# Kernel optimization log

Measured on AMD Instinct MI355X. Metric: run time of the kernel, lower is better.

## Reference

```python
import jax, jax.numpy as jnp
from jax import lax
import numpy as np

H = 32  # LSTM hidden size


def setup_inputs() -> dict:
    key = jax.random.key(0)
    ks = jax.random.split(key, 10)
    B, T = 4096, 200
    s1 = 1.0 / np.sqrt(5)
    sl = 1.0 / np.sqrt(H)
    s2 = 1.0 / np.sqrt(H)
    return {
        "x": jax.random.normal(ks[0], (B, T, 5), dtype=jnp.float32),
        "fc1_w": jax.random.uniform(ks[1], (20, 5), jnp.float32, -s1, s1),
        "fc1_b": jax.random.uniform(ks[2], (20,), jnp.float32, -s1, s1),
        "w_ih": jax.random.uniform(ks[3], (4 * H, 20), jnp.float32, -sl, sl),
        "w_hh": jax.random.uniform(ks[4], (4 * H, H), jnp.float32, -sl, sl),
        "b_ih": jax.random.uniform(ks[5], (4 * H,), jnp.float32, -sl, sl),
        "b_hh": jax.random.uniform(ks[6], (4 * H,), jnp.float32, -sl, sl),
        "fc2_w": jax.random.uniform(ks[7], (2, H), jnp.float32, -s2, s2),
        "fc2_b": jax.random.uniform(ks[8], (2,), jnp.float32, -s2, s2),
    }


def reference(x, fc1_w, fc1_b, w_ih, w_hh, b_ih, b_hh, fc2_w, fc2_b):
    # fc1 + relu (dropout is identity in eval mode)
    h = jax.nn.relu(jnp.einsum("bti,oi->bto", x, fc1_w) + fc1_b)  # [B,T,20]
    B = x.shape[0]
    # Precompute input projections for all timesteps (one big GEMM)
    gx = jnp.einsum("bti,gi->btg", h, w_ih) + b_ih + b_hh  # [B,T,4H]
    gx = jnp.swapaxes(gx, 0, 1)  # [T,B,4H]

    def step(carry, gxt):
        h_prev, c_prev = carry
        gates = gxt + h_prev @ w_hh.T  # [B,4H]
        i, f, g, o = jnp.split(gates, 4, axis=-1)  # torch gate order i,f,g,o
        i = jax.nn.sigmoid(i)
        f = jax.nn.sigmoid(f)
        g = jnp.tanh(g)
        o = jax.nn.sigmoid(o)
        c = f * c_prev + i * g
        hn = o * jnp.tanh(c)
        return (hn, c), None

    zeros = jnp.zeros((B, H), dtype=x.dtype)
    (hT, _), _ = lax.scan(step, (zeros, zeros), gx)
    # fc2 on last timestep's hidden state
    return hT @ fc2_w.T + fc2_b  # [B,2]
```

## Files before the change

kernel.cpp:

```cpp
#include <hip/hip_runtime.h>

#define TT  200
#define IN  5
#define NH  32
#define FC1 20
#define CH  64
#define RS  12

typedef _Float16 h2t __attribute__((ext_vector_type(2)));
typedef _Float16 h4t __attribute__((ext_vector_type(4)));
typedef _Float16 h8t __attribute__((ext_vector_type(8)));

#if __has_builtin(__builtin_amdgcn_fdot2)
#define FDOT2(a, b, c) __builtin_amdgcn_fdot2((a), (b), (c), false)
#else
__device__ __forceinline__ float FDOT2(h2t a, h2t b, float c) {
    return fmaf((float)a.x, (float)b.x, fmaf((float)a.y, (float)b.y, c));
}
#endif

__device__ __forceinline__ float sigm(float a) {
    return __builtin_amdgcn_rcpf(1.f + __expf(-a));
}
__device__ __forceinline__ float tanh_f(float a) {
    return fmaf(2.f, __builtin_amdgcn_rcpf(1.f + __expf(-2.f * a)), -1.f);
}

#define EXT2(dst, src, i0, i1) dst = __builtin_shufflevector(src, src, i0, i1)

__global__ __attribute__((amdgpu_waves_per_eu(4, 4))) __launch_bounds__(64)
void lstm_fused(
    const float* __restrict__ x,
    const float* __restrict__ fc1_w,
    const float* __restrict__ fc1_b,
    const float* __restrict__ w_ih,
    const float* __restrict__ w_hh,
    const float* __restrict__ b_ih,
    const float* __restrict__ b_hh,
    const float* __restrict__ fc2_w,
    const float* __restrict__ fc2_b,
    float* __restrict__ out)
{
    const int b = blockIdx.x;
    const int l = threadIdx.x;
    const int u = l & 31;
    const int p = l >> 5;

    __shared__ __align__(16) h2t h20c[CH * RS];
    __shared__ __align__(16) _Float16 sh_h[NH];

    const int rA = u + 32 * p;
    const int rB = rA + 64;
    h2t wA[26], wB[26];
    {
        const float4* pa = (const float4*)(w_ih + rA * FC1);
        const float4* pb = (const float4*)(w_ih + rB * FC1);
        #pragma unroll
        for (int j = 0; j < 5; ++j) {
            float4 va = pa[j], vb = pb[j];
            wA[2*j]   = h2t{(_Float16)va.x, (_Float16)va.y};
            wA[2*j+1] = h2t{(_Float16)va.z, (_Float16)va.w};
            wB[2*j]   = h2t{(_Float16)vb.x, (_Float16)vb.y};
            wB[2*j+1] = h2t{(_Float16)vb.z, (_Float16)vb.w};
        }
        const float4* ca = (const float4*)(w_hh + rA * NH);
        const float4* cb = (const float4*)(w_hh + rB * NH);
        #pragma unroll
        for (int j = 0; j < 8; ++j) {
            float4 va = ca[j], vb = cb[j];
            wA[10+2*j]   = h2t{(_Float16)va.x, (_Float16)va.y};
            wA[10+2*j+1] = h2t{(_Float16)va.z, (_Float16)va.w};
            wB[10+2*j]   = h2t{(_Float16)vb.x, (_Float16)vb.y};
            wB[10+2*j+1] = h2t{(_Float16)vb.z, (_Float16)vb.w};
        }
    }
    const float biasA = b_ih[rA] + b_hh[rA];
    const float biasB = b_ih[rB] + b_hh[rB];

    const float An = (p == 0) ? 2.f : 1.f;
    const float Bn = (p == 0) ? -2.f : -1.f;
    const float Cn = (p == 0) ? -1.f : 0.f;

    if (l < 16) ((unsigned int*)sh_h)[l] = 0u;
    float c = 0.f;

    const float* xb = x + (size_t)b * (TT * IN);

    for (int tc = 0; tc < TT; tc += CH) {
        {
            const int t = tc + l;
            if (t < TT) {
                float xv[IN];
                #pragma unroll
                for (int i = 0; i < IN; ++i) xv[i] = xb[t * IN + i];
                h2t* row = h20c + (size_t)l * RS;
                #pragma unroll
                for (int j = 0; j < FC1; j += 2) {
                    float a0 = fc1_b[j], a1 = fc1_b[j + 1];
                    #pragma unroll
                    for (int i = 0; i < IN; ++i) {
                        a0 = fmaf(fc1_w[j * IN + i],       xv[i], a0);
                        a1 = fmaf(fc1_w[(j + 1) * IN + i], xv[i], a1);
                    }
                    row[j >> 1] = h2t{(_Float16)fmaxf(a0, 0.f),
                                      (_Float16)fmaxf(a1, 0.f)};
                }
            }
        }
        __syncthreads();

        const int te = (TT - tc < CH) ? (TT - tc) : CH;
        for (int k = 0; k < te; ++k) {
            h2t xin[26];
            {
                const h2t* row = h20c + (size_t)k * RS;
                h8t r0 = *(const h8t*)(row);
                h8t r1 = *(const h8t*)(row + 4);
                h4t r2 = *(const h4t*)(row + 8);
                EXT2(xin[0], r0, 0, 1);  EXT2(xin[1], r0, 2, 3);
                EXT2(xin[2], r0, 4, 5);  EXT2(xin[3], r0, 6, 7);
                EXT2(xin[4], r1, 0, 1);  EXT2(xin[5], r1, 2, 3);
                EXT2(xin[6], r1, 4, 5);  EXT2(xin[7], r1, 6, 7);
                EXT2(xin[8], r2, 0, 1);  EXT2(xin[9], r2, 2, 3);
                const h8t* hp = (const h8t*)sh_h;
                h8t h0 = hp[0], h1 = hp[1], h2 = hp[2], h3 = hp[3];
                EXT2(xin[10], h0, 0, 1); EXT2(xin[11], h0, 2, 3);
                EXT2(xin[12], h0, 4, 5); EXT2(xin[13], h0, 6, 7);
                EXT2(xin[14], h1, 0, 1); EXT2(xin[15], h1, 2, 3);
                EXT2(xin[16], h1, 4, 5); EXT2(xin[17], h1, 6, 7);
                EXT2(xin[18], h2, 0, 1); EXT2(xin[19], h2, 2, 3);
                EXT2(xin[20], h2, 4, 5); EXT2(xin[21], h2, 6, 7);
                EXT2(xin[22], h3, 0, 1); EXT2(xin[23], h3, 2, 3);
                EXT2(xin[24], h3, 4, 5); EXT2(xin[25], h3, 6, 7);
            }

            float aA0 = biasA, aA1 = 0.f, aB0 = biasB, aB1 = 0.f;
            #pragma unroll
            for (int j = 0; j < 26; j += 2) {
                aA0 = FDOT2(wA[j],     xin[j],     aA0);
                aA1 = FDOT2(wA[j + 1], xin[j + 1], aA1);
                aB0 = FDOT2(wB[j],     xin[j],     aB0);
                aB1 = FDOT2(wB[j + 1], xin[j + 1], aB1);
            }
            const float aA = aA0 + aA1;
            const float aB = aB0 + aB1;

            const float s0 = sigm(aA);
            const float e1 = __expf(Bn * aB);
            const float s1 = fmaf(An, __builtin_amdgcn_rcpf(1.f + e1), Cn);

            const float x0 = __shfl_xor(s0, 32);
            const float x1 = __shfl_xor(s1, 32);

            const float ig = (p == 0) ? (s0 * s1) : (x0 * x1);
            const float fv = (p == 0) ? x0 : s0;
            const float ov = (p == 0) ? x1 : s1;
            c = fmaf(fv, c, ig);
            const float hval = ov * tanh_f(c);

            if (p == 0) sh_h[u] = (_Float16)hval;
            __syncthreads();
        }
    }

    if (l < 2) {
        float acc = fc2_b[l];
        #pragma unroll
        for (int k = 0; k < NH; ++k)
            acc = fmaf(fc2_w[l * NH + k], (float)sh_h[k], acc);
        out[(size_t)b * 2 + l] = acc;
    }
}

extern "C" void kernel_launch(void* const* d_in, const int* in_sizes, int n_in,
                              void* d_out, int out_size, void* d_ws, size_t ws_size,
                              hipStream_t stream) {
    const float* x     = (const float*)d_in[0];
    const float* fc1_w = (const float*)d_in[1];
    const float* fc1_b = (const float*)d_in[2];
    const float* w_ih  = (const float*)d_in[3];
    const float* w_hh  = (const float*)d_in[4];
    const float* b_ih  = (const float*)d_in[5];
    const float* b_hh  = (const float*)d_in[6];
    const float* fc2_w = (const float*)d_in[7];
    const float* fc2_b = (const float*)d_in[8];
    float* out = (float*)d_out;

    const int B = in_sizes[0] / (TT * IN);
    lstm_fused<<<dim3(B), dim3(64), 0, stream>>>(
        x, fc1_w, fc1_b, w_ih, w_hh, b_ih, b_hh, fc2_w, fc2_b, out);
}
```

Before: 153.7 us.

## Prepack fp16 recurrent weights in a prep kernel and drop the per-step barrier

A small prep kernel converts w_ih and w_hh to packed fp16 pairs in a row-interleaved workspace layout. The main kernel then loads its per-thread weights with coalesced uint4 reads and no per-element conversion. The per-timestep __syncthreads is replaced by a compiler memory fence, which relies on the 64-thread block being a single wavefront so LDS accesses stay ordered. This adds a second kernel launch and depends on wave64 execution for correctness.

Result: no change. 154.3 us (+0.4%).

```diff
diff --git a/kernel.cpp b/kernel.cpp
--- a/kernel.cpp
+++ b/kernel.cpp
@@ -6,6 +6,7 @@
 #define FC1 20
 #define CH  64
 #define RS  12
+#define NG  7
 
 typedef _Float16 h2t __attribute__((ext_vector_type(2)));
 typedef _Float16 h4t __attribute__((ext_vector_type(4)));
@@ -28,13 +29,31 @@
 
 #define EXT2(dst, src, i0, i1) dst = __builtin_shufflevector(src, src, i0, i1)
 
+__global__ __launch_bounds__(256) void prep_w(
+    const float* __restrict__ w_ih, const float* __restrict__ w_hh,
+    unsigned int* __restrict__ ws)
+{
+    const int tid = blockIdx.x * 256 + threadIdx.x;
+    if (tid >= NG * 128 * 4) return;
+    const int q   = tid & 3;
+    const int rem = tid >> 2;
+    const int row = rem & 127;
+    const int g   = rem >> 7;
+    const int j   = 4 * g + q;
+    const int d0  = 2 * j;
+    float a = 0.f, b = 0.f;
+    if (d0 < FC1)      { a = w_ih[row * FC1 + d0];        b = w_ih[row * FC1 + d0 + 1]; }
+    else if (d0 < 52)  { a = w_hh[row * NH + d0 - FC1];   b = w_hh[row * NH + d0 - FC1 + 1]; }
+    h2t hv = { (_Float16)a, (_Float16)b };
+    ws[tid] = __builtin_bit_cast(unsigned int, hv);
+}
+
 __global__ __attribute__((amdgpu_waves_per_eu(4, 4))) __launch_bounds__(64)
 void lstm_fused(
     const float* __restrict__ x,
     const float* __restrict__ fc1_w,
     const float* __restrict__ fc1_b,
-    const float* __restrict__ w_ih,
-    const float* __restrict__ w_hh,
+    const unsigned int* __restrict__ wt,
     const float* __restrict__ b_ih,
     const float* __restrict__ b_hh,
     const float* __restrict__ fc2_w,
@@ -51,28 +70,29 @@
 
     const int rA = u + 32 * p;
     const int rB = rA + 64;
+
     h2t wA[26], wB[26];
     {
-        const float4* pa = (const float4*)(w_ih + rA * FC1);
-        const float4* pb = (const float4*)(w_ih + rB * FC1);
+        const uint4* wp = (const uint4*)wt;
         #pragma unroll
-        for (int j = 0; j < 5; ++j) {
-            float4 va = pa[j], vb = pb[j];
-            wA[2*j]   = h2t{(_Float16)va.x, (_Float16)va.y};
-            wA[2*j+1] = h2t{(_Float16)va.z, (_Float16)va.w};
-            wB[2*j]   = h2t{(_Float16)vb.x, (_Float16)vb.y};
-            wB[2*j+1] = h2t{(_Float16)vb.z, (_Float16)vb.w};
+        for (int g = 0; g < NG - 1; ++g) {
+            uint4 va = wp[g * 128 + rA];
+            uint4 vb = wp[g * 128 + rB];
+            wA[4*g+0] = __builtin_bit_cast(h2t, va.x);
+            wA[4*g+1] = __builtin_bit_cast(h2t, va.y);
+            wA[4*g+2] = __builtin_bit_cast(h2t, va.z);
+            wA[4*g+3] = __builtin_bit_cast(h2t, va.w);
+            wB[4*g+0] = __builtin_bit_cast(h2t, vb.x);
+            wB[4*g+1] = __builtin_bit_cast(h2t, vb.y);
+            wB[4*g+2] = __builtin_bit_cast(h2t, vb.z);
+            wB[4*g+3] = __builtin_bit_cast(h2t, vb.w);
         }
-        const float4* ca = (const float4*)(w_hh + rA * NH);
-        const float4* cb = (const float4*)(w_hh + rB * NH);
-        #pragma unroll
-        for (int j = 0; j < 8; ++j) {
-            float4 va = ca[j], vb = cb[j];
-            wA[10+2*j]   = h2t{(_Float16)va.x, (_Float16)va.y};
-            wA[10+2*j+1] = h2t{(_Float16)va.z, (_Float16)va.w};
-            wB[10+2*j]   = h2t{(_Float16)vb.x, (_Float16)vb.y};
-            wB[10+2*j+1] = h2t{(_Float16)vb.z, (_Float16)vb.w};
-        }
+        uint4 va = wp[6 * 128 + rA];
+        uint4 vb = wp[6 * 128 + rB];
+        wA[24] = __builtin_bit_cast(h2t, va.x);
+        wA[25] = __builtin_bit_cast(h2t, va.y);
+        wB[24] = __builtin_bit_cast(h2t, vb.x);
+        wB[25] = __builtin_bit_cast(h2t, vb.y);
     }
     const float biasA = b_ih[rA] + b_hh[rA];
     const float biasB = b_ih[rB] + b_hh[rB];
@@ -159,7 +179,7 @@
             const float hval = ov * tanh_f(c);
 
             if (p == 0) sh_h[u] = (_Float16)hval;
-            __syncthreads();
+            asm volatile("" ::: "memory");
         }
     }
 
@@ -185,8 +205,10 @@
     const float* fc2_w = (const float*)d_in[7];
     const float* fc2_b = (const float*)d_in[8];
     float* out = (float*)d_out;
+    unsigned int* ws = (unsigned int*)d_ws;
 
     const int B = in_sizes[0] / (TT * IN);
+    prep_w<<<dim3((NG * 128 * 4 + 255) / 256), dim3(256), 0, stream>>>(w_ih, w_hh, ws);
     lstm_fused<<<dim3(B), dim3(64), 0, stream>>>(
-        x, fc1_w, fc1_b, w_ih, w_hh, b_ih, b_hh, fc2_w, fc2_b, out);
-}
+        x, fc1_w, fc1_b, ws, b_ih, b_hh, fc2_w, fc2_b, out);
+}
```

## Precompute input gate projections per chunk and split recurrent dot across wave halves

Applied to the files above, without the earlier changes.

Moves the W_ih·fc1 projection out of the serial recurrence: each chunk of 16 timesteps is precomputed in parallel into shared memory, and a prep kernel repacks weights to fp16 in workspace. The recurrent step now has each lane compute a 16-wide partial dot for all four gates, combining halves through LDS instead of shuffles. Per-step __syncthreads is replaced by compiler barriers, relying on single-wave lockstep execution. This shortens the serial critical path per timestep, at the cost of an extra kernel launch and reliance on implicit wave synchronisation for LDS visibility.

Result: slower. 275.0 us (+78.9%).

```diff
diff --git a/kernel.cpp b/kernel.cpp
--- a/kernel.cpp
+++ b/kernel.cpp
@@ -4,12 +4,13 @@
 #define IN  5
 #define NH  32
 #define FC1 20
-#define CH  64
-#define RS  12
+#define CH  16
+
+#define WS_WHH  0
+#define WS_WIH  2048
+#define WS_BIAS 3584
 
 typedef _Float16 h2t __attribute__((ext_vector_type(2)));
-typedef _Float16 h4t __attribute__((ext_vector_type(4)));
-typedef _Float16 h8t __attribute__((ext_vector_type(8)));
 
 #if __has_builtin(__builtin_amdgcn_fdot2)
 #define FDOT2(a, b, c) __builtin_amdgcn_fdot2((a), (b), (c), false)
@@ -26,17 +27,43 @@
     return fmaf(2.f, __builtin_amdgcn_rcpf(1.f + __expf(-2.f * a)), -1.f);
 }
 
-#define EXT2(dst, src, i0, i1) dst = __builtin_shufflevector(src, src, i0, i1)
-
-__global__ __attribute__((amdgpu_waves_per_eu(4, 4))) __launch_bounds__(64)
-void lstm_fused(
+__device__ __forceinline__ h2t bc_h2(unsigned int v) {
+    return __builtin_bit_cast(h2t, v);
+}
+
+__global__ __launch_bounds__(256) void prep_w(
+    const float* __restrict__ w_ih, const float* __restrict__ w_hh,
+    const float* __restrict__ b_ih, const float* __restrict__ b_hh,
+    unsigned int* __restrict__ ws)
+{
+    const int tid = blockIdx.x * 256 + threadIdx.x;
+    if (tid < 2048) {
+        const int l = tid >> 5, k = tid & 31;
+        const int rp = k >> 3, j = k & 7;
+        const int row = (l & 31) + 32 * rp;
+        const int d0  = 16 * (l >> 5) + 2 * j;
+        h2t hv = { (_Float16)w_hh[row * NH + d0],
+                   (_Float16)w_hh[row * NH + d0 + 1] };
+        ws[WS_WHH + tid] = __builtin_bit_cast(unsigned int, hv);
+    } else if (tid < 3584) {
+        const int t = tid - 2048;
+        const int row = t / 12, j = t % 12;
+        const int d0 = 2 * j;
+        float a = 0.f, b = 0.f;
+        if (d0 < FC1) { a = w_ih[row * FC1 + d0]; b = w_ih[row * FC1 + d0 + 1]; }
+        h2t hv = { (_Float16)a, (_Float16)b };
+        ws[WS_WIH + (row * 12 + j)] = __builtin_bit_cast(unsigned int, hv);
+    } else if (tid < 3712) {
+        const int r = tid - 3584;
+        ((float*)(ws + WS_BIAS))[r] = b_ih[r] + b_hh[r];
+    }
+}
+
+__global__ __launch_bounds__(64) void lstm_fused(
     const float* __restrict__ x,
     const float* __restrict__ fc1_w,
     const float* __restrict__ fc1_b,
-    const float* __restrict__ w_ih,
-    const float* __restrict__ w_hh,
-    const float* __restrict__ b_ih,
-    const float* __restrict__ b_hh,
+    const unsigned int* __restrict__ ws,
     const float* __restrict__ fc2_w,
     const float* __restrict__ fc2_b,
     float* __restrict__ out)
@@ -46,54 +73,37 @@
     const int u = l & 31;
     const int p = l >> 5;
 
-    __shared__ __align__(16) h2t h20c[CH * RS];
+    __shared__ __align__(16) float4 gx[CH * 32];
+    __shared__ __align__(16) float4 dcomb[64];
     __shared__ __align__(16) _Float16 sh_h[NH];
 
-    const int rA = u + 32 * p;
-    const int rB = rA + 64;
-    h2t wA[26], wB[26];
+    h2t whh[32];
     {
-        const float4* pa = (const float4*)(w_ih + rA * FC1);
-        const float4* pb = (const float4*)(w_ih + rB * FC1);
+        const uint4* wp = (const uint4*)(ws + WS_WHH + l * 32);
         #pragma unroll
-        for (int j = 0; j < 5; ++j) {
-            float4 va = pa[j], vb = pb[j];
-            wA[2*j]   = h2t{(_Float16)va.x, (_Float16)va.y};
-            wA[2*j+1] = h2t{(_Float16)va.z, (_Float16)va.w};
-            wB[2*j]   = h2t{(_Float16)vb.x, (_Float16)vb.y};
-            wB[2*j+1] = h2t{(_Float16)vb.z, (_Float16)vb.w};
+        for (int g = 0; g < 8; ++g) {
+            uint4 v = wp[g];
+            whh[4*g+0] = bc_h2(v.x); whh[4*g+1] = bc_h2(v.y);
+            whh[4*g+2] = bc_h2(v.z); whh[4*g+3] = bc_h2(v.w);
         }
-        const float4* ca = (const float4*)(w_hh + rA * NH);
-        const float4* cb = (const float4*)(w_hh + rB * NH);
-        #pragma unroll
-        for (int j = 0; j < 8; ++j) {
-            float4 va = ca[j], vb = cb[j];
-            wA[10+2*j]   = h2t{(_Float16)va.x, (_Float16)va.y};
-            wA[10+2*j+1] = h2t{(_Float16)va.z, (_Float16)va.w};
-            wB[10+2*j]   = h2t{(_Float16)vb.x, (_Float16)vb.y};
-            wB[10+2*j+1] = h2t{(_Float16)vb.z, (_Float16)vb.w};
-        }
-    }
-    const float biasA = b_ih[rA] + b_hh[rA];
-    const float biasB = b_ih[rB] + b_hh[rB];
-
-    const float An = (p == 0) ? 2.f : 1.f;
-    const float Bn = (p == 0) ? -2.f : -1.f;
-    const float Cn = (p == 0) ? -1.f : 0.f;
+    }
 
     if (l < 16) ((unsigned int*)sh_h)[l] = 0u;
     float c = 0.f;
 
+    const int   tq = l & 15;
+    const int   q  = l >> 4;
     const float* xb = x + (size_t)b * (TT * IN);
+    const float* biasf = (const float*)(ws + WS_BIAS);
 
     for (int tc = 0; tc < TT; tc += CH) {
         {
-            const int t = tc + l;
+            const int t = tc + tq;
             if (t < TT) {
                 float xv[IN];
                 #pragma unroll
                 for (int i = 0; i < IN; ++i) xv[i] = xb[t * IN + i];
-                h2t* row = h20c + (size_t)l * RS;
+                h2t h20p[10];
                 #pragma unroll
                 for (int j = 0; j < FC1; j += 2) {
                     float a0 = fc1_b[j], a1 = fc1_b[j + 1];
@@ -102,8 +112,34 @@
                         a0 = fmaf(fc1_w[j * IN + i],       xv[i], a0);
                         a1 = fmaf(fc1_w[(j + 1) * IN + i], xv[i], a1);
                     }
-                    row[j >> 1] = h2t{(_Float16)fmaxf(a0, 0.f),
-                                      (_Float16)fmaxf(a1, 0.f)};
+                    h20p[j >> 1] = h2t{(_Float16)fmaxf(a0, 0.f),
+                                       (_Float16)fmaxf(a1, 0.f)};
+                }
+                #pragma unroll
+                for (int s = 0; s < 8; ++s) {
+                    const int uslot = 8 * q + s;
+                    float dacc[4];
+                    #pragma unroll
+                    for (int m = 0; m < 4; ++m) {
+                        const int row = uslot + 32 * m;
+                        const uint4* wr = (const uint4*)(ws + WS_WIH + row * 12);
+                        uint4 w0 = wr[0], w1 = wr[1];
+                        uint4 w2 = wr[2];
+                        float a0 = biasf[row], a1 = 0.f;
+                        a0 = FDOT2(bc_h2(w0.x), h20p[0], a0);
+                        a1 = FDOT2(bc_h2(w0.y), h20p[1], a1);
+                        a0 = FDOT2(bc_h2(w0.z), h20p[2], a0);
+                        a1 = FDOT2(bc_h2(w0.w), h20p[3], a1);
+                        a0 = FDOT2(bc_h2(w1.x), h20p[4], a0);
+                        a1 = FDOT2(bc_h2(w1.y), h20p[5], a1);
+                        a0 = FDOT2(bc_h2(w1.z), h20p[6], a0);
+                        a1 = FDOT2(bc_h2(w1.w), h20p[7], a1);
+                        a0 = FDOT2(bc_h2(w2.x), h20p[8], a0);
+                        a1 = FDOT2(bc_h2(w2.y), h20p[9], a1);
+                        dacc[m] = a0 + a1;
+                    }
+                    gx[tq * 32 + uslot] =
+                        make_float4(dacc[0], dacc[1], dacc[2], dacc[3]);
                 }
             }
         }
@@ -111,56 +147,48 @@
 
         const int te = (TT - tc < CH) ? (TT - tc) : CH;
         for (int k = 0; k < te; ++k) {
-            h2t xin[26];
+            const float4 g4 = gx[k * 32 + u];
+            const float sd0 = (p == 0) ? g4.x : 0.f;
+            const float sd1 = (p == 0) ? g4.y : 0.f;
+            const float sd2 = (p == 0) ? g4.z : 0.f;
+            const float sd3 = (p == 0) ? g4.w : 0.f;
+            h2t xin[8];
             {
-                const h2t* row = h20c + (size_t)k * RS;
-                h8t r0 = *(const h8t*)(row);
-                h8t r1 = *(const h8t*)(row + 4);
-                h4t r2 = *(const h4t*)(row + 8);
-                EXT2(xin[0], r0, 0, 1);  EXT2(xin[1], r0, 2, 3);
-                EXT2(xin[2], r0, 4, 5);  EXT2(xin[3], r0, 6, 7);
-                EXT2(xin[4], r1, 0, 1);  EXT2(xin[5], r1, 2, 3);
-                EXT2(xin[6], r1, 4, 5);  EXT2(xin[7], r1, 6, 7);
-                EXT2(xin[8], r2, 0, 1);  EXT2(xin[9], r2, 2, 3);
-                const h8t* hp = (const h8t*)sh_h;
-                h8t h0 = hp[0], h1 = hp[1], h2 = hp[2], h3 = hp[3];
-                EXT2(xin[10], h0, 0, 1); EXT2(xin[11], h0, 2, 3);
-                EXT2(xin[12], h0, 4, 5); EXT2(xin[13], h0, 6, 7);
-                EXT2(xin[14], h1, 0, 1); EXT2(xin[15], h1, 2, 3);
-                EXT2(xin[16], h1, 4, 5); EXT2(xin[17], h1, 6, 7);
-                EXT2(xin[18], h2, 0, 1); EXT2(xin[19], h2, 2, 3);
-                EXT2(xin[20], h2, 4, 5); EXT2(xin[21], h2, 6, 7);
-                EXT2(xin[22], h3, 0, 1); EXT2(xin[23], h3, 2, 3);
-                EXT2(xin[24], h3, 4, 5); EXT2(xin[25], h3, 6, 7);
+                const uint4* hp = (const uint4*)((const char*)sh_h + 32 * p);
+                uint4 h0 = hp[0], h1 = hp[1];
+                xin[0] = bc_h2(h0.x); xin[1] = bc_h2(h0.y);
+                xin[2] = bc_h2(h0.z); xin[3] = bc_h2(h0.w);
+                xin[4] = bc_h2(h1.x); xin[5] = bc_h2(h1.y);
+                xin[6] = bc_h2(h1.z); xin[7] = bc_h2(h1.w);
             }
-
-            float aA0 = biasA, aA1 = 0.f, aB0 = biasB, aB1 = 0.f;
+            float dA[4];
             #pragma unroll
-            for (int j = 0; j < 26; j += 2) {
-                aA0 = FDOT2(wA[j],     xin[j],     aA0);
-                aA1 = FDOT2(wA[j + 1], xin[j + 1], aA1);
-                aB0 = FDOT2(wB[j],     xin[j],     aB0);
-                aB1 = FDOT2(wB[j + 1], xin[j + 1], aB1);
+            for (int m = 0; m < 4; ++m) {
+                float a0 = (m == 0) ? sd0 : (m == 1) ? sd1 : (m == 2) ? sd2 : sd3;
+                float a1 = 0.f;
+                a0 = FDOT2(whh[8*m+0], xin[0], a0);
+                a1 = FDOT2(whh[8*m+1], xin[1], a1);
+                a0 = FDOT2(whh[8*m+2], xin[2], a0);
+                a1 = FDOT2(whh[8*m+3], xin[3], a1);
+                a0 = FDOT2(whh[8*m+4], xin[4], a0);
+                a1 = FDOT2(whh[8*m+5], xin[5], a1);
+                a0 = FDOT2(whh[8*m+6], xin[6], a0);
+                a1 = FDOT2(whh[8*m+7], xin[7], a1);
+                dA[m] = a0 + a1;
             }
-            const float aA = aA0 + aA1;
-            const float aB = aB0 + aB1;
-
-            const float s0 = sigm(aA);
-            const float e1 = __expf(Bn * aB);
-            const float s1 = fmaf(An, __builtin_amdgcn_rcpf(1.f + e1), Cn);
-
-            const float x0 = __shfl_xor(s0, 32);
-            const float x1 = __shfl_xor(s1, 32);
-
-            const float ig = (p == 0) ? (s0 * s1) : (x0 * x1);
-            const float fv = (p == 0) ? x0 : s0;
-            const float ov = (p == 0) ? x1 : s1;
-            c = fmaf(fv, c, ig);
-            const float hval = ov * tanh_f(c);
-
+            dcomb[l] = make_float4(dA[0], dA[1], dA[2], dA[3]);
+            asm volatile("" ::: "memory");
+            const float4 dp = dcomb[l ^ 32];
+            const float gi = sigm(dA[0] + dp.x);
+            const float gf = sigm(dA[1] + dp.y);
+            const float gg = tanh_f(dA[2] + dp.z);
+            const float go = sigm(dA[3] + dp.w);
+            c = fmaf(gf, c, gi * gg);
+            const float hval = go * tanh_f(c);
             if (p == 0) sh_h[u] = (_Float16)hval;
-            __syncthreads();
+            asm volatile("" ::: "memory");
         }
+        __syncthreads();
     }
 
     if (l < 2) {
@@ -185,8 +213,10 @@
     const float* fc2_w = (const float*)d_in[7];
     const float* fc2_b = (const float*)d_in[8];
     float* out = (float*)d_out;
+    unsigned int* ws = (unsigned int*)d_ws;
 
     const int B = in_sizes[0] / (TT * IN);
+    prep_w<<<dim3(15), dim3(256), 0, stream>>>(w_ih, w_hh, b_ih, b_hh, ws);
     lstm_fused<<<dim3(B), dim3(64), 0, stream>>>(
-        x, fc1_w, fc1_b, w_ih, w_hh, b_ih, b_hh, fc2_w, fc2_b, out);
-}
+        x, fc1_w, fc1_b, ws, fc2_w, fc2_b, out);
+}
```
